# Optimization experiments

Hardware: AMD Instinct MI355X
Metric: run time of the kernel (lower is better)

The kernel has to match this reference:

```python
import jax, jax.numpy as jnp
import numpy as np

N_TOKENS = 16384
D_MODEL = 2048
N_EXPERTS = 64
TOP_K = 8
TAU = 1.0
HYSTERESIS = 0.1
LAMBDA_TAX = 0.04
ALPHA_DAMPING = 0.7
SINKHORN_ITERS = 10


def setup_inputs() -> dict:
    key = jax.random.key(0)
    kx, kw, kb, kp, km = jax.random.split(key, 5)
    x = jax.random.normal(kx, (N_TOKENS, D_MODEL), dtype=jnp.float32)
    # LazyLinear(n_experts): weight [E, D], bias [E]
    W = jax.random.normal(kw, (N_EXPERTS, D_MODEL), dtype=jnp.float32) * (1.0 / np.sqrt(D_MODEL))
    b = jax.random.normal(kb, (N_EXPERTS,), dtype=jnp.float32) * 0.01
    # prev_probs buffer: a valid probability distribution per token
    prev_probs = jax.nn.softmax(jax.random.normal(kp, (N_TOKENS, N_EXPERTS), dtype=jnp.float32), axis=-1)
    # prev_mask buffer: exactly k experts active per token (what forward produces)
    scores = jax.random.normal(km, (N_TOKENS, N_EXPERTS), dtype=jnp.float32)
    idx = jax.lax.top_k(scores, TOP_K)[1]
    prev_mask = jnp.zeros((N_TOKENS, N_EXPERTS), dtype=bool).at[jnp.arange(N_TOKENS)[:, None], idx].set(True)
    return {"x": x, "W": W, "b": b, "prev_probs": prev_probs, "prev_mask": prev_mask}


def _router_probs(x, W, b, prev_probs, prev_mask):
    n = x.shape[0]
    logits = x @ W.T + b                               # [N, E]
    logits = logits - jnp.mean(logits, axis=-1, keepdims=True)
    M = jax.nn.softmax(logits / TAU, axis=-1)
    # Exact analytical gradient correction (correlation tax)
    C = M.T @ M                                        # [E, E]
    C = C * (1.0 - jnp.eye(N_EXPERTS, dtype=C.dtype))  # fill_diagonal_(0)
    grad_m = 4.0 * (M @ C)
    exact_grad = M * grad_m - M * jnp.sum(M * grad_m, axis=-1, keepdims=True)
    logits = logits - LAMBDA_TAX * exact_grad
    M = jax.nn.softmax(logits / TAU, axis=-1)
    # Convergent Sinkhorn-Knopp (10 fixed iterations)
    def body(i, M):
        M = M / jnp.clip(jnp.sum(M, axis=0, keepdims=True), 1e-12)
        M = M * (N_EXPERTS / n)
        M = M / jnp.clip(jnp.sum(M, axis=1, keepdims=True), 1e-12)
        return M
    M = jax.lax.fori_loop(0, SINKHORN_ITERS, body, M)
    # Momental damping with previous probs
    M = (1.0 - ALPHA_DAMPING) * prev_probs + ALPHA_DAMPING * M
    # Hysteresis blend with previous mask
    prev = prev_mask.astype(M.dtype)
    denom = jnp.clip(jnp.sum(prev, axis=-1, keepdims=True), 1.0)
    M = (1.0 - HYSTERESIS) * M + HYSTERESIS * (prev / denom)
    M = M / jnp.clip(jnp.sum(M, axis=-1, keepdims=True), 1e-12)
    return M


def reference(x, W, b, prev_probs, prev_mask):
    M = _router_probs(x, W, b, prev_probs, prev_mask)
    idx = jax.lax.top_k(M, TOP_K)[1]                   # [N, k]
    n = M.shape[0]
    mask = jnp.zeros(M.shape, dtype=bool).at[jnp.arange(n)[:, None], idx].set(True)
    return M, mask
```

## Files before the change

### kernel.cpp

```cpp
#include <hip/hip_runtime.h>
#include <math.h>

#define NT 16384
#define DM 2048
#define NE 64
#define TOPK 8
#define LTAX 0.04f
#define HYST 0.1f
#define ALPHA 0.7f

typedef unsigned int u32;
typedef unsigned short u16;
typedef unsigned long long u64;
typedef __attribute__((ext_vector_type(8))) short bf16x8;
typedef __attribute__((ext_vector_type(4))) float f32x4;

__device__ __forceinline__ float warp4_sum(float v) {
  v += __shfl_xor(v, 1); v += __shfl_xor(v, 2); return v;
}
__device__ __forceinline__ float warp4_max(float v) {
  v = fmaxf(v, __shfl_xor(v, 1)); v = fmaxf(v, __shfl_xor(v, 2)); return v;
}
__device__ __forceinline__ u16 f2bf(float f) {
  u32 u = __float_as_uint(f);
  return (u16)((u + 0x7fffu + ((u >> 16) & 1u)) >> 16);
}
__device__ __forceinline__ float bf2f(u16 h) { return __uint_as_float(((u32)h) << 16); }

__device__ __forceinline__ void split3(float a, short& h, short& m, short& l) {
  u16 hh = f2bf(a);  float r1 = a - bf2f(hh);
  u16 mm = f2bf(r1); float r2 = r1 - bf2f(mm);
  h = (short)hh; m = (short)mm; l = (short)f2bf(r2);
}

__device__ __forceinline__ u64 to_fx(float v) {
  return (u64)__double2ll_rn((double)v * 4294967296.0);
}

__global__ void k_wsplit3(const float* __restrict__ W, u16* __restrict__ Wh,
                          u16* __restrict__ Wm, u16* __restrict__ Wl) {
  int idx = (blockIdx.x * 256 + threadIdx.x) * 4;
  float4 v = *(const float4*)(W + idx);
  short h[4], m[4], l[4];
  split3(v.x, h[0], m[0], l[0]);
  split3(v.y, h[1], m[1], l[1]);
  split3(v.z, h[2], m[2], l[2]);
  split3(v.w, h[3], m[3], l[3]);
  *(ushort4*)(Wh + idx) = make_ushort4((u16)h[0], (u16)h[1], (u16)h[2], (u16)h[3]);
  *(ushort4*)(Wm + idx) = make_ushort4((u16)m[0], (u16)m[1], (u16)m[2], (u16)m[3]);
  *(ushort4*)(Wl + idx) = make_ushort4((u16)l[0], (u16)l[1], (u16)l[2], (u16)l[3]);
}

__launch_bounds__(256, 2)
__global__ void k_gemm(const float* __restrict__ x, const u16* __restrict__ Whg,
                       const u16* __restrict__ Wmg, const u16* __restrict__ Wlg,
                       double* __restrict__ Lpart) {
  __shared__ __align__(16) u16 XS[30720];
  const int tid = threadIdx.x;
  const int bid = blockIdx.x;
  const int tile = bid >> 1, ks = bid & 1;
  const int row0 = tile * 64;
  const int k0 = ks * 1024;
  const int lane = tid & 63, w = tid >> 6, l15 = lane & 15, l4 = lane >> 4;
  const int srow = tid >> 2, c8 = (tid & 3) * 8;
  const int stoff = srow * 40 + c8;

  f32x4 accA[4], accB[4];
  double accD[4][4];
#pragma unroll
  for (int eb = 0; eb < 4; eb++) {
    accA[eb] = (f32x4)0.f; accB[eb] = (f32x4)0.f;
#pragma unroll
    for (int r = 0; r < 4; r++) accD[eb][r] = 0.0;
  }

  float4 xq0, xq1;
  uint4 whv, wmv, wlv;
  const float* xrowp = x + (size_t)(row0 + srow) * DM + k0 + c8;
  const u16* whp = Whg + srow * DM + k0 + c8;
  const u16* wmp = Wmg + srow * DM + k0 + c8;
  const u16* wlp = Wlg + srow * DM + k0 + c8;

#define LOADCH(KC) { \
    xq0 = *(const float4*)(xrowp + (KC)); \
    xq1 = *(const float4*)(xrowp + (KC) + 4); \
    whv = *(const uint4*)(whp + (KC)); \
    wmv = *(const uint4*)(wmp + (KC)); \
    wlv = *(const uint4*)(wlp + (KC)); }

#define WRITECH(B) { \
    short ha[8], ma[8], la[8]; \
    split3(xq0.x, ha[0], ma[0], la[0]); \
    split3(xq0.y, ha[1], ma[1], la[1]); \
    split3(xq0.z, ha[2], ma[2], la[2]); \
    split3(xq0.w, ha[3], ma[3], la[3]); \
    split3(xq1.x, ha[4], ma[4], la[4]); \
    split3(xq1.y, ha[5], ma[5], la[5]); \
    split3(xq1.z, ha[6], ma[6], la[6]); \
    split3(xq1.w, ha[7], ma[7], la[7]); \
    bf16x8 xh8, xm8, xl8; \
    _Pragma("unroll") \
    for (int z = 0; z < 8; z++) { xh8[z] = ha[z]; xm8[z] = ma[z]; xl8[z] = la[z]; } \
    *(bf16x8*)(XS + 0     + (B) * 2560 + stoff) = xh8; \
    *(bf16x8*)(XS + 5120  + (B) * 2560 + stoff) = xm8; \
    *(bf16x8*)(XS + 10240 + (B) * 2560 + stoff) = xl8; \
    *(uint4*)(XS + 15360 + (B) * 2560 + stoff) = whv; \
    *(uint4*)(XS + 20480 + (B) * 2560 + stoff) = wmv; \
    *(uint4*)(XS + 25600 + (B) * 2560 + stoff) = wlv; }

#define COMPUTECH(B) { \
    const int ar = (w * 16 + l15) * 40 + l4 * 8; \
    bf16x8 ah = *(const bf16x8*)(XS + 0     + (B) * 2560 + ar); \
    bf16x8 am = *(const bf16x8*)(XS + 5120  + (B) * 2560 + ar); \
    bf16x8 al = *(const bf16x8*)(XS + 10240 + (B) * 2560 + ar); \
    _Pragma("unroll") \
    for (int eb = 0; eb < 4; eb++) { \
      const int br = (eb * 16 + l15) * 40 + l4 * 8; \
      bf16x8 bh = *(const bf16x8*)(XS + 15360 + (B) * 2560 + br); \
      bf16x8 bm = *(const bf16x8*)(XS + 20480 + (B) * 2560 + br); \
      bf16x8 bl = *(const bf16x8*)(XS + 25600 + (B) * 2560 + br); \
      accA[eb] = __builtin_amdgcn_mfma_f32_16x16x32_bf16(ah, bh, accA[eb], 0, 0, 0); \
      accB[eb] = __builtin_amdgcn_mfma_f32_16x16x32_bf16(ah, bm, accB[eb], 0, 0, 0); \
      accB[eb] = __builtin_amdgcn_mfma_f32_16x16x32_bf16(am, bh, accB[eb], 0, 0, 0); \
      accB[eb] = __builtin_amdgcn_mfma_f32_16x16x32_bf16(am, bm, accB[eb], 0, 0, 0); \
      accB[eb] = __builtin_amdgcn_mfma_f32_16x16x32_bf16(ah, bl, accB[eb], 0, 0, 0); \
      accB[eb] = __builtin_amdgcn_mfma_f32_16x16x32_bf16(al, bh, accB[eb], 0, 0, 0); \
    } }

  LOADCH(0);
  WRITECH(0);
  __syncthreads();
#pragma unroll 1
  for (int t = 0; t < 32; t++) {
    if (t < 31) LOADCH((t + 1) * 32);
    COMPUTECH(t & 1);
    if ((t & 7) == 7) {
#pragma unroll
      for (int eb = 0; eb < 4; eb++) {
#pragma unroll
        for (int r = 0; r < 4; r++)
          accD[eb][r] += (double)accA[eb][r] + (double)accB[eb][r];
        accA[eb] = (f32x4)0.f; accB[eb] = (f32x4)0.f;
      }
    }
    if (t < 31) WRITECH((t + 1) & 1);
    __syncthreads();
  }

  double* outp = Lpart + (size_t)ks * NT * NE;
#pragma unroll
  for (int eb = 0; eb < 4; eb++)
#pragma unroll
    for (int r = 0; r < 4; r++) {
      int trow = w * 16 + l4 * 4 + r;
      outp[(size_t)(row0 + trow) * NE + eb * 16 + l15] = accD[eb][r];
    }
}

__launch_bounds__(256)
__global__ void k_post(const double* __restrict__ Lpart, const float* __restrict__ b,
                       float* __restrict__ Lbuf, u64* __restrict__ CmAcc) {
  __shared__ float ms[64 * 68];
  const int tid = threadIdx.x, bid = blockIdx.x;
  const int tg = tid >> 2, q = tid & 3;
  const int row = bid * 64 + tg;
  float l[16], m[16];
  {
    const double* p0 = Lpart + (size_t)row * NE + q * 16;
    const double* p1 = p0 + (size_t)NT * NE;
#pragma unroll
    for (int i = 0; i < 4; i++) {
      float4 bv = *(const float4*)(b + q * 16 + i * 4);
      l[i * 4 + 0] = (float)(p0[i * 4 + 0] + p1[i * 4 + 0]) + bv.x;
      l[i * 4 + 1] = (float)(p0[i * 4 + 1] + p1[i * 4 + 1]) + bv.y;
      l[i * 4 + 2] = (float)(p0[i * 4 + 2] + p1[i * 4 + 2]) + bv.z;
      l[i * 4 + 3] = (float)(p0[i * 4 + 3] + p1[i * 4 + 3]) + bv.w;
    }
    float s = 0.f;
#pragma unroll
    for (int j = 0; j < 16; j++) s += l[j];
    s = warp4_sum(s);
    const float mean = s * (1.0f / 64.0f);
    float mx = -1e30f;
#pragma unroll
    for (int j = 0; j < 16; j++) { l[j] -= mean; mx = fmaxf(mx, l[j]); }
    mx = warp4_max(mx);
#pragma unroll
    for (int i = 0; i < 4; i++)
      *(float4*)(Lbuf + (size_t)row * NE + q * 16 + i * 4) =
          make_float4(l[i * 4], l[i * 4 + 1], l[i * 4 + 2], l[i * 4 + 3]);
    float ps = 0.f;
#pragma unroll
    for (int j = 0; j < 16; j++) { m[j] = expf(l[j] - mx); ps += m[j]; }
    ps = warp4_sum(ps);
    const float inv = 1.0f / ps;
#pragma unroll
    for (int j = 0; j < 16; j++) m[j] *= inv;
#pragma unroll
    for (int i = 0; i < 4; i++)
      *(float4*)(ms + tg * 68 + q * 16 + i * 4) =
          make_float4(m[i * 4], m[i * 4 + 1], m[i * 4 + 2], m[i * 4 + 3]);
  }
  __syncthreads();
  const int gi0 = (tid >> 4) * 4;
  const int gj0 = (tid & 15) * 4;
  float ga[4][4];
#pragma unroll
  for (int a = 0; a < 4; a++)
#pragma unroll
    for (int c = 0; c < 4; c++) ga[a][c] = 0.f;
  for (int t = 0; t < 64; t++) {
    float4 a = *(const float4*)(ms + t * 68 + gi0);
    float4 bb = *(const float4*)(ms + t * 68 + gj0);
    ga[0][0] = fmaf(a.x, bb.x, ga[0][0]); ga[0][1] = fmaf(a.x, bb.y, ga[0][1]);
    ga[0][2] = fmaf(a.x, bb.z, ga[0][2]); ga[0][3] = fmaf(a.x, bb.w, ga[0][3]);
    ga[1][0] = fmaf(a.y, bb.x, ga[1][0]); ga[1][1] = fmaf(a.y, bb.y, ga[1][1]);
    ga[1][2] = fmaf(a.y, bb.z, ga[1][2]); ga[1][3] = fmaf(a.y, bb.w, ga[1][3]);
    ga[2][0] = fmaf(a.z, bb.x, ga[2][0]); ga[2][1] = fmaf(a.z, bb.y, ga[2][1]);
    ga[2][2] = fmaf(a.z, bb.z, ga[2][2]); ga[2][3] = fmaf(a.z, bb.w, ga[2][3]);
    ga[3][0] = fmaf(a.w, bb.x, ga[3][0]); ga[3][1] = fmaf(a.w, bb.y, ga[3][1]);
    ga[3][2] = fmaf(a.w, bb.z, ga[3][2]); ga[3][3] = fmaf(a.w, bb.w, ga[3][3]);
  }
  u64* slot = CmAcc + (size_t)(bid & 3) * 4096;
#pragma unroll
  for (int ii = 0; ii < 4; ii++)
#pragma unroll
    for (int jj = 0; jj < 4; jj++)
      atomicAdd(slot + (gi0 + ii) * 64 + gj0 + jj, to_fx(ga[ii][jj]));
}

__launch_bounds__(256)
__global__ void k_correct(const float* __restrict__ Lbuf, const u64* __restrict__ CmAcc,
                          float* __restrict__ M0, u64* __restrict__ p0Acc) {
  __shared__ float ms[64 * 68];
  __shared__ float Cs[4096];
  __shared__ float cred[256];
  const int tid = threadIdx.x, bid = blockIdx.x;
  const int tg = tid >> 2, q = tid & 3;
  const int lane = tid & 63, w = tid >> 6;
  const int row = bid * 64 + tg;
  float l[16], m[16];
#pragma unroll
  for (int i = 0; i < 4; i++) {
    float4 lv = *(const float4*)(Lbuf + (size_t)row * NE + q * 16 + i * 4);
    l[i * 4 + 0] = lv.x; l[i * 4 + 1] = lv.y; l[i * 4 + 2] = lv.z; l[i * 4 + 3] = lv.w;
  }
  {
    float mx = -1e30f;
#pragma unroll
    for (int j = 0; j < 16; j++) mx = fmaxf(mx, l[j]);
    mx = warp4_max(mx);
    float ps = 0.f;
#pragma unroll
    for (int j = 0; j < 16; j++) { m[j] = expf(l[j] - mx); ps += m[j]; }
    ps = warp4_sum(ps);
    const float inv = 1.0f / ps;
#pragma unroll
    for (int j = 0; j < 16; j++) m[j] *= inv;
#pragma unroll
    for (int i = 0; i < 4; i++)
      *(float4*)(ms + tg * 68 + q * 16 + i * 4) =
          make_float4(m[i * 4], m[i * 4 + 1], m[i * 4 + 2], m[i * 4 + 3]);
  }
#pragma unroll 4
  for (int i = 0; i < 16; i++) {
    int idx = tid + i * 256;
    u64 s = CmAcc[idx] + CmAcc[4096 + idx] + CmAcc[8192 + idx] + CmAcc[12288 + idx];
    float v = (float)((double)s * (1.0 / 4294967296.0));
    int r = idx >> 6, c = idx & 63;
    Cs[idx] = (r == c) ? 0.f : v;
  }
  __syncthreads();
  {
    float g[16];
#pragma unroll
    for (int j = 0; j < 16; j++) g[j] = 0.f;
    for (int f = 0; f < 64; f++) {
      float mf = ms[tg * 68 + f];
#pragma unroll
      for (int i = 0; i < 4; i++) {
        float4 cv = *(const float4*)(Cs + f * 64 + q * 16 + i * 4);
        g[i * 4 + 0] = fmaf(mf, cv.x, g[i * 4 + 0]);
        g[i * 4 + 1] = fmaf(mf, cv.y, g[i * 4 + 1]);
        g[i * 4 + 2] = fmaf(mf, cv.z, g[i * 4 + 2]);
        g[i * 4 + 3] = fmaf(mf, cv.w, g[i * 4 + 3]);
      }
    }
    float dot = 0.f;
#pragma unroll
    for (int j = 0; j < 16; j++) { g[j] *= 4.f; dot += m[j] * g[j]; }
    dot = warp4_sum(dot);
    float mx = -1e30f;
#pragma unroll
    for (int j = 0; j < 16; j++) {
      l[j] = l[j] - LTAX * (m[j] * (g[j] - dot));
      mx = fmaxf(mx, l[j]);
    }
    mx = warp4_max(mx);
    float ps = 0.f;
#pragma unroll
    for (int j = 0; j < 16; j++) { m[j] = expf(l[j] - mx); ps += m[j]; }
    ps = warp4_sum(ps);
    const float inv = 1.0f / ps;
#pragma unroll
    for (int j = 0; j < 16; j++) m[j] *= inv;
#pragma unroll
    for (int i = 0; i < 4; i++)
      *(float4*)(M0 + (size_t)row * NE + q * 16 + i * 4) =
          make_float4(m[i * 4], m[i * 4 + 1], m[i * 4 + 2], m[i * 4 + 3]);
  }
  {
    float cs[16];
#pragma unroll
    for (int j = 0; j < 16; j++) cs[j] = m[j];
#pragma unroll
    for (int j = 0; j < 16; j++) {
      cs[j] += __shfl_xor(cs[j], 4);  cs[j] += __shfl_xor(cs[j], 8);
      cs[j] += __shfl_xor(cs[j], 16); cs[j] += __shfl_xor(cs[j], 32);
    }
    if ((lane >> 2) == 0) {
#pragma unroll
      for (int j = 0; j < 16; j++) cred[w * 64 + lane * 16 + j] = cs[j];
    }
    __syncthreads();
    if (tid < 64)
      atomicAdd(p0Acc + (size_t)(bid & 15) * 64 + tid,
                to_fx(cred[tid] + cred[64 + tid] + cred[128 + tid] + cred[192 + tid]));
  }
}

__launch_bounds__(256)
__global__ void k_sink(const float* __restrict__ M0, const u64* __restrict__ pin,
                       u64* __restrict__ pout) {
  __shared__ float fac[64];
  __shared__ float cred[256];
  const int tid = threadIdx.x, bid = blockIdx.x;
  const int tg = tid >> 2, q = tid & 3;
  const int lane = tid & 63, w = tid >> 6;
  const int row = bid * 64 + tg;
  if (tid < 64) {
    u64 s = 0;
#pragma unroll
    for (int sl = 0; sl < 16; sl++) s += pin[sl * 64 + tid];
    float P = (float)((double)s * (1.0 / 4294967296.0));
    fac[tid] = 256.0f / fmaxf(P, 1e-30f);
  }
  __syncthreads();
  float mv[16];
#pragma unroll
  for (int i = 0; i < 4; i++) {
    float4 v = *(const float4*)(M0 + (size_t)row * NE + q * 16 + i * 4);
    mv[i * 4 + 0] = v.x; mv[i * 4 + 1] = v.y; mv[i * 4 + 2] = v.z; mv[i * 4 + 3] = v.w;
  }
  float Q = 0.f;
#pragma unroll
  for (int j = 0; j < 16; j++) Q = fmaf(mv[j], fac[q * 16 + j], Q);
  Q = warp4_sum(Q);
  const float U = 1.0f / fmaxf(Q, 1e-30f);
  float cs[16];
#pragma unroll
  for (int j = 0; j < 16; j++) cs[j] = U * mv[j];
#pragma unroll
  for (int j = 0; j < 16; j++) {
    cs[j] += __shfl_xor(cs[j], 4);  cs[j] += __shfl_xor(cs[j], 8);
    cs[j] += __shfl_xor(cs[j], 16); cs[j] += __shfl_xor(cs[j], 32);
  }
  if ((lane >> 2) == 0) {
#pragma unroll
    for (int j = 0; j < 16; j++) cred[w * 64 + lane * 16 + j] = cs[j];
  }
  __syncthreads();
  if (tid < 64)
    atomicAdd(pout + (size_t)(bid & 15) * 64 + tid,
              to_fx(cred[tid] + cred[64 + tid] + cred[128 + tid] + cred[192 + tid]));
}

__launch_bounds__(256)
__global__ void k_final(const float* __restrict__ M0, const u64* __restrict__ pin,
                        const float* __restrict__ pp, const void* __restrict__ pmask,
                        float* __restrict__ out) {
  __shared__ float fac[64];
  __shared__ int s_cnt[256];
  __shared__ int s_flag;
  const int tid = threadIdx.x, bid = blockIdx.x;
  const int tg = tid >> 2, q = tid & 3;
  const int lane = tid & 63;
  const int row = bid * 64 + tg;

  {
    uint4 v = ((const uint4*)pmask)[tid];
    int c = 0; u32 ww;
    ww = v.x; c += ((ww & 0xffu) != 0) + ((ww & 0xff00u) != 0) + ((ww & 0xff0000u) != 0) + ((ww & 0xff000000u) != 0);
    ww = v.y; c += ((ww & 0xffu) != 0) + ((ww & 0xff00u) != 0) + ((ww & 0xff0000u) != 0) + ((ww & 0xff000000u) != 0);
    ww = v.z; c += ((ww & 0xffu) != 0) + ((ww & 0xff00u) != 0) + ((ww & 0xff0000u) != 0) + ((ww & 0xff000000u) != 0);
    ww = v.w; c += ((ww & 0xffu) != 0) + ((ww & 0xff00u) != 0) + ((ww & 0xff0000u) != 0) + ((ww & 0xff000000u) != 0);
    s_cnt[tid] = c;
    __syncthreads();
    for (int s = 128; s; s >>= 1) { if (tid < s) s_cnt[tid] += s_cnt[tid + s]; __syncthreads(); }
    if (tid == 0) { int n = s_cnt[0]; s_flag = (n > 384) ? 0 : ((n > 192) ? 2 : 1); }
  }
  if (tid < 64) {
    u64 s = 0;
#pragma unroll
    for (int sl = 0; sl < 16; sl++) s += pin[sl * 64 + tid];
    float P = (float)((double)s * (1.0 / 4294967296.0));
    fac[tid] = 256.0f / fmaxf(P, 1e-30f);
  }
  __syncthreads();

  float mv[16];
#pragma unroll
  for (int i = 0; i < 4; i++) {
    float4 v = *(const float4*)(M0 + (size_t)row * NE + q * 16 + i * 4);
    mv[i * 4 + 0] = v.x; mv[i * 4 + 1] = v.y; mv[i * 4 + 2] = v.z; mv[i * 4 + 3] = v.w;
  }
  float Q = 0.f;
#pragma unroll
  for (int j = 0; j < 16; j++) Q = fmaf(mv[j], fac[q * 16 + j], Q);
  Q = warp4_sum(Q);
  const float U = 1.0f / fmaxf(Q, 1e-30f);
  float m[16];
#pragma unroll
  for (int j = 0; j < 16; j++) m[j] = U * mv[j] * fac[q * 16 + j];

  const int flag = s_flag;
  float pv[16], mk[16];
#pragma unroll
  for (int i = 0; i < 4; i++) {
    float4 v = *(const float4*)(pp + (size_t)row * NE + q * 16 + i * 4);
    pv[i * 4 + 0] = v.x; pv[i * 4 + 1] = v.y; pv[i * 4 + 2] = v.z; pv[i * 4 + 3] = v.w;
  }
  if (flag == 0) {
    const u32* pb = (const u32*)pmask + row * 16 + q * 4;
#pragma unroll
    for (int i = 0; i < 4; i++) {
      u32 ww = pb[i];
      mk[i * 4 + 0] = (ww & 0xffu) ? 1.f : 0.f;
      mk[i * 4 + 1] = (ww & 0xff00u) ? 1.f : 0.f;
      mk[i * 4 + 2] = (ww & 0xff0000u) ? 1.f : 0.f;
      mk[i * 4 + 3] = (ww & 0xff000000u) ? 1.f : 0.f;
    }
  } else if (flag == 1) {
    const int* pb = (const int*)pmask + (size_t)row * NE + q * 16;
#pragma unroll
    for (int j = 0; j < 16; j++) mk[j] = pb[j] ? 1.f : 0.f;
  } else {
    const float* pb = (const float*)pmask + (size_t)row * NE + q * 16;
#pragma unroll
    for (int j = 0; j < 16; j++) mk[j] = (pb[j] != 0.f) ? 1.f : 0.f;
  }
  float msum = 0.f;
#pragma unroll
  for (int j = 0; j < 16; j++) msum += mk[j];
  msum = warp4_sum(msum);
  const float hscale = HYST / fmaxf(msum, 1.0f);
  float v[16];
  float s = 0.f;
#pragma unroll
  for (int j = 0; j < 16; j++) {
    float base = (1.f - ALPHA) * pv[j] + ALPHA * m[j];
    v[j] = (1.f - HYST) * base + hscale * mk[j];
    s += v[j];
  }
  s = warp4_sum(s);
  const float inv = 1.0f / fmaxf(s, 1e-12f);
#pragma unroll
  for (int j = 0; j < 16; j++) v[j] *= inv;

  float* mout = out;
  float* kout = out + (size_t)NT * NE;
#pragma unroll
  for (int i = 0; i < 4; i++)
    *(float4*)(mout + (size_t)row * NE + q * 16 + i * 4) =
        make_float4(v[i * 4], v[i * 4 + 1], v[i * 4 + 2], v[i * 4 + 3]);

  int cnt[16];
#pragma unroll
  for (int j = 0; j < 16; j++) cnt[j] = 0;
  const int base = lane & ~3;
#pragma unroll
  for (int oq = 0; oq < 4; oq++) {
#pragma unroll
    for (int j2 = 0; j2 < 16; j2++) {
      float ov = __shfl(v[j2], base + oq, 64);
      int oe = oq * 16 + j2;
#pragma unroll
      for (int j = 0; j < 16; j++) {
        int me = q * 16 + j;
        if (ov > v[j] || (ov == v[j] && oe < me)) cnt[j]++;
      }
    }
  }
#pragma unroll
  for (int i = 0; i < 4; i++)
    *(float4*)(kout + (size_t)row * NE + q * 16 + i * 4) =
        make_float4(cnt[i * 4] < TOPK ? 1.f : 0.f, cnt[i * 4 + 1] < TOPK ? 1.f : 0.f,
                    cnt[i * 4 + 2] < TOPK ? 1.f : 0.f, cnt[i * 4 + 3] < TOPK ? 1.f : 0.f);
}

extern "C" void kernel_launch(void* const* d_in, const int* in_sizes, int n_in,
                              void* d_out, int out_size, void* d_ws, size_t ws_size,
                              hipStream_t stream) {
  const float* x = (const float*)d_in[0];
  const float* W = (const float*)d_in[1];
  const float* b = (const float*)d_in[2];
  const float* pp = (const float*)d_in[3];
  const void* pmask = d_in[4];
  float* out = (float*)d_out;

  unsigned char* wsb = (unsigned char*)d_ws;
  u16* Wh = (u16*)(wsb);
  u16* Wm = (u16*)(wsb + 262144);
  u16* Wl = (u16*)(wsb + 524288);
  double* Lpart = (double*)(wsb + 786432);
  float* Lbuf = (float*)(wsb + 17563648);
  float* M0buf = (float*)(wsb + 21757952);
  u64* CmAcc = (u64*)(wsb + 25952256);
  u64* pAcc = (u64*)(wsb + 26083328);

  hipMemsetAsync(wsb + 25952256, 0, 212992, stream);
  k_wsplit3<<<128, 256, 0, stream>>>(W, Wh, Wm, Wl);
  k_gemm<<<512, 256, 0, stream>>>(x, Wh, Wm, Wl, Lpart);
  k_post<<<256, 256, 0, stream>>>(Lpart, b, Lbuf, CmAcc);
  k_correct<<<256, 256, 0, stream>>>(Lbuf, CmAcc, M0buf, pAcc);
  for (int k = 1; k <= 9; k++)
    k_sink<<<256, 256, 0, stream>>>(M0buf, pAcc + (size_t)(k - 1) * 1024,
                                    pAcc + (size_t)k * 1024);
  k_final<<<256, 256, 0, stream>>>(M0buf, pAcc + (size_t)9 * 1024, pp, pmask, out);
}
```

Measured before the change: 181.3 us.

## Fuse GEMM with post-processing, drop split-K and memset into init kernel

Merges the logits GEMM and the softmax/correlation post kernel into one kernel. Each block now covers the full K=2048 for 64 rows instead of splitting K across two blocks, so the double-precision partial logits never go to global memory. The workspace memset is folded into the W-split kernel, and the 16-slot partial-sum reads in the Sinkhorn and final kernels are spread across all threads. The cost is that the GEMM grid drops from 512 to 256 blocks at one block per SM, so fewer CUs get work and each block runs longer.

```diff
diff --git a/kernel.cpp b/kernel.cpp
--- a/kernel.cpp
+++ b/kernel.cpp
@@ -37,30 +37,36 @@
   return (u64)__double2ll_rn((double)v * 4294967296.0);
 }
 
-__global__ void k_wsplit3(const float* __restrict__ W, u16* __restrict__ Wh,
-                          u16* __restrict__ Wm, u16* __restrict__ Wl) {
-  int idx = (blockIdx.x * 256 + threadIdx.x) * 4;
-  float4 v = *(const float4*)(W + idx);
-  short h[4], m[4], l[4];
-  split3(v.x, h[0], m[0], l[0]);
-  split3(v.y, h[1], m[1], l[1]);
-  split3(v.z, h[2], m[2], l[2]);
-  split3(v.w, h[3], m[3], l[3]);
-  *(ushort4*)(Wh + idx) = make_ushort4((u16)h[0], (u16)h[1], (u16)h[2], (u16)h[3]);
-  *(ushort4*)(Wm + idx) = make_ushort4((u16)m[0], (u16)m[1], (u16)m[2], (u16)m[3]);
-  *(ushort4*)(Wl + idx) = make_ushort4((u16)l[0], (u16)l[1], (u16)l[2], (u16)l[3]);
-}
-
-__launch_bounds__(256, 2)
-__global__ void k_gemm(const float* __restrict__ x, const u16* __restrict__ Whg,
-                       const u16* __restrict__ Wmg, const u16* __restrict__ Wlg,
-                       double* __restrict__ Lpart) {
+__global__ void k_init(const float* __restrict__ W, u16* __restrict__ Wh,
+                       u16* __restrict__ Wm, u16* __restrict__ Wl,
+                       u64* __restrict__ zp) {
+  const int bid = blockIdx.x, tid = threadIdx.x;
+  if (bid < 128) {
+    int idx = (bid * 256 + tid) * 4;
+    float4 v = *(const float4*)(W + idx);
+    short h[4], m[4], l[4];
+    split3(v.x, h[0], m[0], l[0]);
+    split3(v.y, h[1], m[1], l[1]);
+    split3(v.z, h[2], m[2], l[2]);
+    split3(v.w, h[3], m[3], l[3]);
+    *(ushort4*)(Wh + idx) = make_ushort4((u16)h[0], (u16)h[1], (u16)h[2], (u16)h[3]);
+    *(ushort4*)(Wm + idx) = make_ushort4((u16)m[0], (u16)m[1], (u16)m[2], (u16)m[3]);
+    *(ushort4*)(Wl + idx) = make_ushort4((u16)l[0], (u16)l[1], (u16)l[2], (u16)l[3]);
+  } else {
+    int i = (bid - 128) * 256 + tid;
+    if (i < 26624) zp[i] = 0ull;
+  }
+}
+
+__launch_bounds__(256, 1)
+__global__ void k_gemmpost(const float* __restrict__ x, const u16* __restrict__ Whg,
+                           const u16* __restrict__ Wmg, const u16* __restrict__ Wlg,
+                           const float* __restrict__ b, float* __restrict__ Lbuf,
+                           u64* __restrict__ CmAcc) {
   __shared__ __align__(16) u16 XS[30720];
   const int tid = threadIdx.x;
   const int bid = blockIdx.x;
-  const int tile = bid >> 1, ks = bid & 1;
-  const int row0 = tile * 64;
-  const int k0 = ks * 1024;
+  const int row0 = bid * 64;
   const int lane = tid & 63, w = tid >> 6, l15 = lane & 15, l4 = lane >> 4;
   const int srow = tid >> 2, c8 = (tid & 3) * 8;
   const int stoff = srow * 40 + c8;
@@ -76,10 +82,10 @@
 
   float4 xq0, xq1;
   uint4 whv, wmv, wlv;
-  const float* xrowp = x + (size_t)(row0 + srow) * DM + k0 + c8;
-  const u16* whp = Whg + srow * DM + k0 + c8;
-  const u16* wmp = Wmg + srow * DM + k0 + c8;
-  const u16* wlp = Wlg + srow * DM + k0 + c8;
+  const float* xrowp = x + (size_t)(row0 + srow) * DM + c8;
+  const u16* whp = Whg + srow * DM + c8;
+  const u16* wmp = Wmg + srow * DM + c8;
+  const u16* wlp = Wlg + srow * DM + c8;
 
 #define LOADCH(KC) { \
     xq0 = *(const float4*)(xrowp + (KC)); \
@@ -131,8 +137,8 @@
   WRITECH(0);
   __syncthreads();
 #pragma unroll 1
-  for (int t = 0; t < 32; t++) {
-    if (t < 31) LOADCH((t + 1) * 32);
+  for (int t = 0; t < 64; t++) {
+    if (t < 63) LOADCH((t + 1) * 32);
     COMPUTECH(t & 1);
     if ((t & 7) == 7) {
 #pragma unroll
@@ -143,65 +149,57 @@
         accA[eb] = (f32x4)0.f; accB[eb] = (f32x4)0.f;
       }
     }
-    if (t < 31) WRITECH((t + 1) & 1);
+    if (t < 63) WRITECH((t + 1) & 1);
     __syncthreads();
   }
 
-  double* outp = Lpart + (size_t)ks * NT * NE;
+  float* ls = (float*)XS;
+  float* ms = (float*)XS + 4352;
 #pragma unroll
   for (int eb = 0; eb < 4; eb++)
 #pragma unroll
     for (int r = 0; r < 4; r++) {
       int trow = w * 16 + l4 * 4 + r;
-      outp[(size_t)(row0 + trow) * NE + eb * 16 + l15] = accD[eb][r];
-    }
-}
-
-__launch_bounds__(256)
-__global__ void k_post(const double* __restrict__ Lpart, const float* __restrict__ b,
-                       float* __restrict__ Lbuf, u64* __restrict__ CmAcc) {
-  __shared__ float ms[64 * 68];
-  const int tid = threadIdx.x, bid = blockIdx.x;
+      ls[trow * 68 + eb * 16 + l15] = (float)accD[eb][r];
+    }
+  __syncthreads();
+
   const int tg = tid >> 2, q = tid & 3;
-  const int row = bid * 64 + tg;
+  const int row = row0 + tg;
   float l[16], m[16];
-  {
-    const double* p0 = Lpart + (size_t)row * NE + q * 16;
-    const double* p1 = p0 + (size_t)NT * NE;
-#pragma unroll
-    for (int i = 0; i < 4; i++) {
-      float4 bv = *(const float4*)(b + q * 16 + i * 4);
-      l[i * 4 + 0] = (float)(p0[i * 4 + 0] + p1[i * 4 + 0]) + bv.x;
-      l[i * 4 + 1] = (float)(p0[i * 4 + 1] + p1[i * 4 + 1]) + bv.y;
-      l[i * 4 + 2] = (float)(p0[i * 4 + 2] + p1[i * 4 + 2]) + bv.z;
-      l[i * 4 + 3] = (float)(p0[i * 4 + 3] + p1[i * 4 + 3]) + bv.w;
-    }
-    float s = 0.f;
-#pragma unroll
-    for (int j = 0; j < 16; j++) s += l[j];
-    s = warp4_sum(s);
-    const float mean = s * (1.0f / 64.0f);
-    float mx = -1e30f;
-#pragma unroll
-    for (int j = 0; j < 16; j++) { l[j] -= mean; mx = fmaxf(mx, l[j]); }
-    mx = warp4_max(mx);
-#pragma unroll
-    for (int i = 0; i < 4; i++)
-      *(float4*)(Lbuf + (size_t)row * NE + q * 16 + i * 4) =
-          make_float4(l[i * 4], l[i * 4 + 1], l[i * 4 + 2], l[i * 4 + 3]);
-    float ps = 0.f;
-#pragma unroll
-    for (int j = 0; j < 16; j++) { m[j] = expf(l[j] - mx); ps += m[j]; }
-    ps = warp4_sum(ps);
-    const float inv = 1.0f / ps;
-#pragma unroll
-    for (int j = 0; j < 16; j++) m[j] *= inv;
-#pragma unroll
-    for (int i = 0; i < 4; i++)
-      *(float4*)(ms + tg * 68 + q * 16 + i * 4) =
-          make_float4(m[i * 4], m[i * 4 + 1], m[i * 4 + 2], m[i * 4 + 3]);
-  }
-  __syncthreads();
+#pragma unroll
+  for (int i = 0; i < 4; i++) {
+    float4 lv = *(const float4*)(ls + tg * 68 + q * 16 + i * 4);
+    float4 bv = *(const float4*)(b + q * 16 + i * 4);
+    l[i * 4 + 0] = lv.x + bv.x; l[i * 4 + 1] = lv.y + bv.y;
+    l[i * 4 + 2] = lv.z + bv.z; l[i * 4 + 3] = lv.w + bv.w;
+  }
+  float s = 0.f;
+#pragma unroll
+  for (int j = 0; j < 16; j++) s += l[j];
+  s = warp4_sum(s);
+  const float mean = s * (1.0f / 64.0f);
+  float mx = -1e30f;
+#pragma unroll
+  for (int j = 0; j < 16; j++) { l[j] -= mean; mx = fmaxf(mx, l[j]); }
+  mx = warp4_max(mx);
+#pragma unroll
+  for (int i = 0; i < 4; i++)
+    *(float4*)(Lbuf + (size_t)row * NE + q * 16 + i * 4) =
+        make_float4(l[i * 4], l[i * 4 + 1], l[i * 4 + 2], l[i * 4 + 3]);
+  float ps = 0.f;
+#pragma unroll
+  for (int j = 0; j < 16; j++) { m[j] = expf(l[j] - mx); ps += m[j]; }
+  ps = warp4_sum(ps);
+  const float inv = 1.0f / ps;
+#pragma unroll
+  for (int j = 0; j < 16; j++) m[j] *= inv;
+#pragma unroll
+  for (int i = 0; i < 4; i++)
+    *(float4*)(ms + tg * 68 + q * 16 + i * 4) =
+        make_float4(m[i * 4], m[i * 4 + 1], m[i * 4 + 2], m[i * 4 + 3]);
+  __syncthreads();
+
   const int gi0 = (tid >> 4) * 4;
   const int gj0 = (tid & 15) * 4;
   float ga[4][4];
@@ -332,16 +330,21 @@
 __launch_bounds__(256)
 __global__ void k_sink(const float* __restrict__ M0, const u64* __restrict__ pin,
                        u64* __restrict__ pout) {
+  __shared__ u64 pred[4][64];
   __shared__ float fac[64];
   __shared__ float cred[256];
   const int tid = threadIdx.x, bid = blockIdx.x;
   const int tg = tid >> 2, q = tid & 3;
   const int lane = tid & 63, w = tid >> 6;
   const int row = bid * 64 + tg;
+  {
+    const int grp = tid >> 6, e = tid & 63;
+    pred[grp][e] = pin[grp * 64 + e] + pin[(grp + 4) * 64 + e] +
+                   pin[(grp + 8) * 64 + e] + pin[(grp + 12) * 64 + e];
+  }
+  __syncthreads();
   if (tid < 64) {
-    u64 s = 0;
-#pragma unroll
-    for (int sl = 0; sl < 16; sl++) s += pin[sl * 64 + tid];
+    u64 s = pred[0][tid] + pred[1][tid] + pred[2][tid] + pred[3][tid];
     float P = (float)((double)s * (1.0 / 4294967296.0));
     fac[tid] = 256.0f / fmaxf(P, 1e-30f);
   }
@@ -379,6 +382,7 @@
 __global__ void k_final(const float* __restrict__ M0, const u64* __restrict__ pin,
                         const float* __restrict__ pp, const void* __restrict__ pmask,
                         float* __restrict__ out) {
+  __shared__ u64 pred[4][64];
   __shared__ float fac[64];
   __shared__ int s_cnt[256];
   __shared__ int s_flag;
@@ -399,10 +403,14 @@
     for (int s = 128; s; s >>= 1) { if (tid < s) s_cnt[tid] += s_cnt[tid + s]; __syncthreads(); }
     if (tid == 0) { int n = s_cnt[0]; s_flag = (n > 384) ? 0 : ((n > 192) ? 2 : 1); }
   }
+  {
+    const int grp = tid >> 6, e = tid & 63;
+    pred[grp][e] = pin[grp * 64 + e] + pin[(grp + 4) * 64 + e] +
+                   pin[(grp + 8) * 64 + e] + pin[(grp + 12) * 64 + e];
+  }
+  __syncthreads();
   if (tid < 64) {
-    u64 s = 0;
-#pragma unroll
-    for (int sl = 0; sl < 16; sl++) s += pin[sl * 64 + tid];
+    u64 s = pred[0][tid] + pred[1][tid] + pred[2][tid] + pred[3][tid];
     float P = (float)((double)s * (1.0 / 4294967296.0));
     fac[tid] = 256.0f / fmaxf(P, 1e-30f);
   }
@@ -512,16 +520,13 @@
   u16* Wh = (u16*)(wsb);
   u16* Wm = (u16*)(wsb + 262144);
   u16* Wl = (u16*)(wsb + 524288);
-  double* Lpart = (double*)(wsb + 786432);
-  float* Lbuf = (float*)(wsb + 17563648);
-  float* M0buf = (float*)(wsb + 21757952);
-  u64* CmAcc = (u64*)(wsb + 25952256);
-  u64* pAcc = (u64*)(wsb + 26083328);
-
-  hipMemsetAsync(wsb + 25952256, 0, 212992, stream);
-  k_wsplit3<<<128, 256, 0, stream>>>(W, Wh, Wm, Wl);
-  k_gemm<<<512, 256, 0, stream>>>(x, Wh, Wm, Wl, Lpart);
-  k_post<<<256, 256, 0, stream>>>(Lpart, b, Lbuf, CmAcc);
+  float* Lbuf = (float*)(wsb + 786432);
+  float* M0buf = (float*)(wsb + 4980736);
+  u64* CmAcc = (u64*)(wsb + 9175040);
+  u64* pAcc = (u64*)(wsb + 9306112);
+
+  k_init<<<232, 256, 0, stream>>>(W, Wh, Wm, Wl, CmAcc);
+  k_gemmpost<<<256, 256, 0, stream>>>(x, Wh, Wm, Wl, b, Lbuf, CmAcc);
   k_correct<<<256, 256, 0, stream>>>(Lbuf, CmAcc, M0buf, pAcc);
   for (int k = 1; k <= 9; k++)
     k_sink<<<256, 256, 0, stream>>>(M0buf, pAcc + (size_t)(k - 1) * 1024,
```

New measurement: 192.8 us. 6.3% more time.
